# Kernel tuning notes

Measured on AMD Instinct MI355X. Metric: run time of the kernel, lower is better.

The kernel has to match this reference:

```python
import jax, jax.numpy as jnp
import numpy as np

N_LEVELS_ACT = 256  # 8-bit activations (q, k, v)
N_LEVELS_W = 256    # 8-bit softmax weights (always_zero: zp=0)
GN_GROUPS = 32
GN_EPS = 1e-6


def round_ste(x):
    # straight-through round (identity grad)
    return x + jax.lax.stop_gradient(jnp.round(x) - x)


def fake_quant(x, delta, zp, n_levels):
    xq = jnp.clip(round_ste(x / delta) + zp, 0.0, n_levels - 1)
    return (xq - zp) * delta


def group_norm(x, gamma, beta):
    b, c, h, w = x.shape
    xg = x.reshape(b, GN_GROUPS, c // GN_GROUPS, h, w)
    mu = jnp.mean(xg, axis=(2, 3, 4), keepdims=True)
    var = jnp.var(xg, axis=(2, 3, 4), keepdims=True)
    xg = (xg - mu) * jax.lax.rsqrt(var + GN_EPS)
    x = xg.reshape(b, c, h, w)
    return x * gamma[None, :, None, None] + beta[None, :, None, None]


def conv1x1(x, w, b):
    # x: [b,c,h,w], w: [out,in]
    return jnp.einsum('oc,bchw->bohw', w, x) + b[None, :, None, None]


def setup_inputs() -> dict:
    key = jax.random.key(0)
    ks = jax.random.split(key, 8)
    B, C, H, W = 4, 512, 64, 64
    s = 1.0 / np.sqrt(C)
    inp = {
        'x': jax.random.normal(ks[0], (B, C, H, W), jnp.float32),
        'gamma': jnp.ones((C,), jnp.float32),
        'beta': jnp.zeros((C,), jnp.float32),
        'wq': jax.random.normal(ks[1], (C, C), jnp.float32) * s,
        'bq': jnp.zeros((C,), jnp.float32),
        'wk': jax.random.normal(ks[2], (C, C), jnp.float32) * s,
        'bk': jnp.zeros((C,), jnp.float32),
        'wv': jax.random.normal(ks[3], (C, C), jnp.float32) * s,
        'bv': jnp.zeros((C,), jnp.float32),
        'wp': jax.random.normal(ks[4], (C, C), jnp.float32) * s,
        'bp': jnp.zeros((C,), jnp.float32),
        # calibrated asymmetric 8-bit ranges ~ [-4, 4] for q/k/v
        'delta_q': jnp.float32(8.0 / 255.0), 'zp_q': jnp.float32(128.0),
        'delta_k': jnp.float32(8.0 / 255.0), 'zp_k': jnp.float32(128.0),
        'delta_v': jnp.float32(8.0 / 255.0), 'zp_v': jnp.float32(128.0),
        # softmax weights in [0,1], always_zero => zp=0, delta = max/(2^b-1)
        'delta_w': jnp.float32(1.0 / 255.0),
    }
    return inp


def reference(x, gamma, beta, wq, bq, wk, bk, wv, bv, wp, bp,
              delta_q, zp_q, delta_k, zp_k, delta_v, zp_v, delta_w):
    b, c, h, w = x.shape
    hn = group_norm(x, gamma, beta)
    q = conv1x1(hn, wq, bq).reshape(b, c, h * w).transpose(0, 2, 1)  # [b,hw,c]
    k = conv1x1(hn, wk, bk).reshape(b, c, h * w)                      # [b,c,hw]
    v = conv1x1(hn, wv, bv).reshape(b, c, h * w)                      # [b,c,hw]
    q = fake_quant(q, delta_q, zp_q, N_LEVELS_ACT)
    k = fake_quant(k, delta_k, zp_k, N_LEVELS_ACT)
    w_ = jnp.einsum('bqc,bck->bqk', q, k) * (float(c) ** -0.5)
    w_ = jax.nn.softmax(w_, axis=2)
    w_ = w_.transpose(0, 2, 1)  # [b,k,q]
    v = fake_quant(v, delta_v, zp_v, N_LEVELS_ACT)
    w_ = fake_quant(w_, delta_w, jnp.float32(0.0), N_LEVELS_W)
    h_ = jnp.einsum('bck,bkq->bcq', v, w_).reshape(b, c, h, w)
    h_ = conv1x1(h_, wp, bp)
    return x + h_
```

## Files before the change

### kernel.cpp

```cpp
#include <hip/hip_runtime.h>
#include <cstdint>
#include <cstddef>

#define B_  4
#define C_  512
#define HW_ 4096

typedef unsigned short u16t;
typedef signed char s8t;
typedef __attribute__((ext_vector_type(8))) __bf16 bf16x8;
typedef __attribute__((ext_vector_type(4))) float  f32x4;
typedef __attribute__((ext_vector_type(4))) int    i32x4;

__device__ __forceinline__ u16t f2bft(float f) {
    return (u16t)(__float_as_uint(f) >> 16);
}
__device__ __forceinline__ float bf2f(u16t h) {
    return __uint_as_float(((unsigned int)h) << 16);
}
__device__ __forceinline__ f32x4 mfma16(bf16x8 a, bf16x8 b, f32x4 c) {
    return __builtin_amdgcn_mfma_f32_16x16x32_bf16(a, b, c, 0, 0, 0);
}
__device__ __forceinline__ i32x4 mfma_i8(i32x4 a, i32x4 b, i32x4 c) {
    return __builtin_amdgcn_mfma_i32_16x16x64_i8(a, b, c, 0, 0, 0);
}
__device__ __forceinline__ void gl16(const void* g, void* l) {
    __builtin_amdgcn_global_load_lds(
        (__attribute__((address_space(1))) unsigned int*)g,
        (__attribute__((address_space(3))) unsigned int*)l, 16, 0, 0);
}

__global__ __launch_bounds__(256) void split_w(
    const float* __restrict__ wq_, const float* __restrict__ wk_,
    const float* __restrict__ wv_, const float* __restrict__ wp_,
    u16t* __restrict__ out)
{
    int i = blockIdx.x * 256 + threadIdx.x;
    int mat = i >> 18, idx = i & 262143;
    const float* src = (mat == 0) ? wq_ : (mat == 1) ? wk_ : (mat == 2) ? wv_ : wp_;
    float v = src[idx];
    u16t hi = f2bft(v);
    u16t lo = f2bft(v - bf2f(hi));
    out[(size_t)mat * 524288 + idx] = hi;
    out[(size_t)mat * 524288 + 262144 + idx] = lo;
}

__global__ __launch_bounds__(1024) void gn_stats(
    const float* __restrict__ x, float2* __restrict__ stats)
{
    const int tid = threadIdx.x;
    const int bg = blockIdx.x;
    const int b = bg >> 5, g = bg & 31;
    const float4* x4 = (const float4*)(x + ((size_t)b * C_ + g * 16) * HW_);
    float s = 0.f, s2 = 0.f;
    for (int i = tid; i < 16384; i += 1024) {
        float4 v = x4[i];
        s  += v.x + v.y + v.z + v.w;
        s2 += v.x * v.x + v.y * v.y + v.z * v.z + v.w * v.w;
    }
    for (int off = 32; off; off >>= 1) { s += __shfl_down(s, off); s2 += __shfl_down(s2, off); }
    __shared__ float rs[16], rs2[16];
    int w = tid >> 6, lane = tid & 63;
    if (lane == 0) { rs[w] = s; rs2[w] = s2; }
    __syncthreads();
    if (tid == 0) {
        float S = 0.f, S2 = 0.f;
        #pragma unroll
        for (int i = 0; i < 16; ++i) { S += rs[i]; S2 += rs2[i]; }
        float mu = S * (1.f / 65536.f);
        float var = S2 * (1.f / 65536.f) - mu * mu;
        stats[bg] = make_float2(mu, 1.f / sqrtf(var + 1e-6f));
    }
}

__global__ __launch_bounds__(256) void gn_apply(
    const float* __restrict__ x, const float* __restrict__ gamma,
    const float* __restrict__ beta, const float2* __restrict__ stats,
    u16t* __restrict__ hn_hi, u16t* __restrict__ hn_lo)
{
    __shared__ unsigned int tile[16 * 529];
    __shared__ float sa[512], sb[512];
    const int tid = threadIdx.x;
    const int b = blockIdx.y, p0 = blockIdx.x * 16;
    for (int c = tid; c < 512; c += 256) {
        float2 st = stats[b * 32 + (c >> 4)];
        float a = st.y * gamma[c];
        sa[c] = a; sb[c] = beta[c] - st.x * a;
    }
    __syncthreads();
    const float4* x4 = (const float4*)(x + (size_t)b * C_ * HW_);
    const int f4 = tid & 3, cb = tid >> 2;
    #pragma unroll
    for (int it = 0; it < 8; ++it) {
        int c = cb + it * 64;
        float4 v = x4[(size_t)c * (HW_ / 4) + (p0 >> 2) + f4];
        float a = sa[c], bo = sb[c];
        float ys[4] = { v.x, v.y, v.z, v.w };
        #pragma unroll
        for (int j = 0; j < 4; ++j) {
            float y = ys[j] * a + bo;
            u16t hi = f2bft(y);
            u16t lo = f2bft(y - bf2f(hi));
            tile[(f4 * 4 + j) * 529 + c] = (unsigned int)hi | ((unsigned int)lo << 16);
        }
    }
    __syncthreads();
    const int p = tid & 15, seg = tid >> 4;
    size_t ro = ((size_t)b * HW_ + p0 + p) * C_;
    #pragma unroll
    for (int gg = 0; gg < 4; ++gg) {
        const unsigned int* src = &tile[p * 529 + seg * 32 + gg * 8];
        uint4 va = *(const uint4*)src;
        uint4 vb = *(const uint4*)(src + 4);
        uint4 hi4, lo4;
        hi4.x = (va.x & 0xFFFFu) | (va.y << 16);
        hi4.y = (va.z & 0xFFFFu) | (va.w << 16);
        hi4.z = (vb.x & 0xFFFFu) | (vb.y << 16);
        hi4.w = (vb.z & 0xFFFFu) | (vb.w << 16);
        lo4.x = (va.x >> 16) | (va.y & 0xFFFF0000u);
        lo4.y = (va.z >> 16) | (va.w & 0xFFFF0000u);
        lo4.z = (vb.x >> 16) | (vb.y & 0xFFFF0000u);
        lo4.w = (vb.z >> 16) | (vb.w & 0xFFFF0000u);
        *(uint4*)(hn_hi + ro + seg * 32 + gg * 8) = hi4;
        *(uint4*)(hn_lo + ro + seg * 32 + gg * 8) = lo4;
    }
}

template<int MODE>
__global__ __launch_bounds__(256) void gemm512(
    const u16t* __restrict__ Ahi, const u16t* __restrict__ Alo,
    const u16t* __restrict__ Bhi, const u16t* __restrict__ Blo,
    const float* __restrict__ bias, const float* __restrict__ delta,
    const float* __restrict__ zp, s8t* __restrict__ outq,
    float* __restrict__ outf, const float* __restrict__ resid)
{
    __shared__ __align__(16) u16t lds[16384];
    const int tid = threadIdx.x, w = tid >> 6, lane = tid & 63;
    const int lr = lane & 15, gq = lane >> 4, wr = w >> 1, wc = w & 1;
    const int m0 = blockIdx.x * 128, n0 = blockIdx.y * 128, b = blockIdx.z;
    const size_t boff = (size_t)b * HW_ * C_;
    const u16t* gsrc = (w == 0) ? Ahi : (w == 1) ? Alo : (w == 2) ? (Bhi + boff) : (Blo + boff);
    const int rb0 = (w < 2) ? m0 : n0;
    u16t* ldst = lds + w * 4096;
    const int srow = lane >> 2, sch = lane & 3;
    const u16t* sAh = lds; const u16t* sAl = lds + 4096;
    const u16t* sBh = lds + 8192; const u16t* sBl = lds + 12288;
    f32x4 acc[4][4] = {};

    for (int kt = 0; kt < 16; ++kt) {
        const u16t* gk = gsrc + (size_t)(rb0 + srow) * C_ + kt * 32 + sch * 8;
        #pragma unroll
        for (int i = 0; i < 8; ++i) gl16(gk + i * 16 * C_, ldst + i * 512);
        __syncthreads();
        bf16x8 ah[4], al[4], bh[4], bl[4];
        #pragma unroll
        for (int m = 0; m < 4; ++m) {
            int r = wr * 64 + m * 16 + lr;
            ah[m] = *(const bf16x8*)(sAh + r * 32 + gq * 8);
            al[m] = *(const bf16x8*)(sAl + r * 32 + gq * 8);
        }
        #pragma unroll
        for (int n = 0; n < 4; ++n) {
            int r = wc * 64 + n * 16 + lr;
            bh[n] = *(const bf16x8*)(sBh + r * 32 + gq * 8);
            bl[n] = *(const bf16x8*)(sBl + r * 32 + gq * 8);
        }
        #pragma unroll
        for (int m = 0; m < 4; ++m)
            #pragma unroll
            for (int n = 0; n < 4; ++n) {
                acc[m][n] = mfma16(ah[m], bh[n], acc[m][n]);
                acc[m][n] = mfma16(ah[m], bl[n], acc[m][n]);
                acc[m][n] = mfma16(al[m], bh[n], acc[m][n]);
            }
        __syncthreads();
    }

    if constexpr (MODE == 0) {
        const float d = *delta, z = *zp;
        const float rd = 1.0f / d;
        char* T8 = (char*)lds;
        #pragma unroll
        for (int m = 0; m < 4; ++m)
            #pragma unroll
            for (int n = 0; n < 4; ++n)
                #pragma unroll
                for (int j = 0; j < 4; ++j) {
                    int row = wr * 64 + m * 16 + gq * 4 + j;
                    int col = wc * 64 + n * 16 + lr;
                    float val = acc[m][n][j] + bias[m0 + row];
                    float q = fminf(fmaxf(rintf(val * rd), -z), 255.f - z);
                    T8[col * 144 + row] = (char)(int)q;
                }
        __syncthreads();
        int pl = tid >> 1, hf = tid & 1;
        uint4* dst = (uint4*)(outq + ((size_t)b * HW_ + n0 + pl) * C_ + m0 + hf * 64);
        const uint4* s4 = (const uint4*)(T8 + pl * 144 + hf * 64);
        #pragma unroll
        for (int i = 0; i < 4; ++i) dst[i] = s4[i];
    } else if constexpr (MODE == 1) {
        const float d = *delta, z = *zp;
        const float rd = 1.0f / d;
        char* T8 = (char*)lds;
        #pragma unroll
        for (int m = 0; m < 4; ++m)
            #pragma unroll
            for (int n = 0; n < 4; ++n)
                #pragma unroll
                for (int j = 0; j < 4; ++j) {
                    int row = wr * 64 + m * 16 + gq * 4 + j;
                    int col = wc * 64 + n * 16 + lr;
                    float val = acc[m][n][j] + bias[m0 + row];
                    float q = fminf(fmaxf(rintf(val * rd), -z), 255.f - z);
                    T8[row * 144 + col] = (char)(int)q;
                }
        __syncthreads();
        int pl = tid >> 1, hf = tid & 1;
        uint4* dst = (uint4*)(outq + ((size_t)b * C_ + m0 + pl) * HW_ + n0 + hf * 64);
        const uint4* s4 = (const uint4*)(T8 + pl * 144 + hf * 64);
        #pragma unroll
        for (int i = 0; i < 4; ++i) dst[i] = s4[i];
    } else {
        #pragma unroll
        for (int m = 0; m < 4; ++m)
            #pragma unroll
            for (int n = 0; n < 4; ++n)
                #pragma unroll
                for (int j = 0; j < 4; ++j) {
                    int row = wr * 64 + m * 16 + gq * 4 + j;
                    int col = wc * 64 + n * 16 + lr;
                    size_t o = ((size_t)b * C_ + m0 + row) * HW_ + n0 + col;
                    outf[o] = acc[m][n][j] + bias[m0 + row] + resid[o];
                }
    }
}

template<int PASS>
__global__ __launch_bounds__(256) void attn_score(
    const s8t* __restrict__ Qt, const s8t* __restrict__ Kt,
    const float* __restrict__ dqp, const float* __restrict__ dkp,
    float2* __restrict__ pml, const float2* __restrict__ ml,
    s8t* __restrict__ W8)
{
    __shared__ __align__(16) char lds[18432];
    __shared__ float redm[256], reds[256];
    const int tid = threadIdx.x, w = tid >> 6, lane = tid & 63;
    const int lr = lane & 15, gq = lane >> 4, wr = w >> 1, wc = w & 1;
    const int m0 = blockIdx.x * 128, n0 = blockIdx.y * 128, b = blockIdx.z;
    const size_t bo = (size_t)b * HW_ * C_;
    const s8t* gsrc = ((w < 2) ? Qt : Kt) + bo;
    const int rb0 = ((w < 2) ? m0 : n0) + (w & 1) * 64;
    char* ldst = lds + ((w < 2) ? 0 : 8192) + (w & 1) * 4096;
    const int srow = lane >> 2, sch = lane & 3;
    i32x4 acc[4][4] = {};

    for (int kt = 0; kt < 8; ++kt) {
        const s8t* gk = gsrc + (size_t)(rb0 + srow) * C_ + kt * 64 + sch * 16;
        #pragma unroll
        for (int i = 0; i < 4; ++i) gl16(gk + (size_t)i * 16 * C_, ldst + i * 1024);
        __syncthreads();
        i32x4 af[4], bf[4];
        #pragma unroll
        for (int m = 0; m < 4; ++m)
            af[m] = *(const i32x4*)(lds + (wr * 64 + m * 16 + lr) * 64 + gq * 16);
        #pragma unroll
        for (int n = 0; n < 4; ++n)
            bf[n] = *(const i32x4*)(lds + 8192 + (wc * 64 + n * 16 + lr) * 64 + gq * 16);
        #pragma unroll
        for (int m = 0; m < 4; ++m)
            #pragma unroll
            for (int n = 0; n < 4; ++n)
                acc[m][n] = mfma_i8(af[m], bf[n], acc[m][n]);
        __syncthreads();
    }

    const float sc = (*dqp) * (*dkp) * 0.044194173824159216f;
    if constexpr (PASS == 0) {
        #pragma unroll
        for (int m = 0; m < 4; ++m)
            #pragma unroll
            for (int j = 0; j < 4; ++j) {
                float v0 = (float)acc[m][0][j] * sc, v1 = (float)acc[m][1][j] * sc;
                float v2 = (float)acc[m][2][j] * sc, v3 = (float)acc[m][3][j] * sc;
                float mx = fmaxf(fmaxf(v0, v1), fmaxf(v2, v3));
                for (int off = 1; off < 16; off <<= 1) mx = fmaxf(mx, __shfl_xor(mx, off));
                float se = __expf(v0 - mx) + __expf(v1 - mx) + __expf(v2 - mx) + __expf(v3 - mx);
                for (int off = 1; off < 16; off <<= 1) se += __shfl_xor(se, off);
                if (lr == 0) {
                    int r = wr * 64 + m * 16 + gq * 4 + j;
                    redm[r * 2 + wc] = mx; reds[r * 2 + wc] = se;
                }
            }
        __syncthreads();
        if (tid < 128) {
            float ma = redm[tid * 2], mb = redm[tid * 2 + 1];
            float mm = fmaxf(ma, mb);
            float ss = reds[tid * 2] * __expf(ma - mm) + reds[tid * 2 + 1] * __expf(mb - mm);
            pml[((size_t)b * HW_ + m0 + tid) * 32 + blockIdx.y] = make_float2(mm, ss);
        }
    } else {
        char* P8 = lds;
        #pragma unroll
        for (int m = 0; m < 4; ++m)
            #pragma unroll
            for (int j = 0; j < 4; ++j) {
                int row = wr * 64 + m * 16 + gq * 4 + j;
                float2 mv = ml[(size_t)b * HW_ + m0 + row];
                #pragma unroll
                for (int n = 0; n < 4; ++n) {
                    int col = wc * 64 + n * 16 + lr;
                    float sv = __builtin_fmaf((float)acc[m][n][j], sc, -mv.x);
                    float r = rintf(__expf(sv) * mv.y);
                    r = fminf(fmaxf(r, 0.f), 255.f);
                    P8[row * 144 + col] = (char)((int)r - 128);
                }
            }
        __syncthreads();
        int pl = tid >> 1, hf = tid & 1;
        uint4* dst = (uint4*)(W8 + ((size_t)b * HW_ + m0 + pl) * HW_ + n0 + hf * 64);
        const uint4* s4 = (const uint4*)(P8 + pl * 144 + hf * 64);
        #pragma unroll
        for (int i = 0; i < 4; ++i) dst[i] = s4[i];
    }
}

__global__ __launch_bounds__(256) void reduce_ml_k(
    const float2* __restrict__ pml, float2* __restrict__ ml,
    const float* __restrict__ dwp)
{
    int idx = blockIdx.x * 256 + threadIdx.x;
    const float2* p = pml + (size_t)idx * 32;
    float2 vv[32];
    float mm = -3.402823466e38f;
    #pragma unroll
    for (int i = 0; i < 32; ++i) { vv[i] = p[i]; mm = fmaxf(mm, vv[i].x); }
    float l = 0.f;
    #pragma unroll
    for (int i = 0; i < 32; ++i) l += vv[i].y * __expf(vv[i].x - mm);
    ml[idx] = make_float2(mm, 1.0f / (l * (*dwp)));
}

__global__ __launch_bounds__(64) void rowsum_v(
    const s8t* __restrict__ V, int* __restrict__ rsum)
{
    const int row = blockIdx.x, lane = threadIdx.x;
    const int4* src = (const int4*)(V + (size_t)row * HW_);
    int s = 0;
    #pragma unroll
    for (int it = 0; it < 4; ++it) {
        int4 v = src[it * 64 + lane];
        int ww[4] = { v.x, v.y, v.z, v.w };
        #pragma unroll
        for (int d = 0; d < 4; ++d) {
            int xv = ww[d];
            s += (int)(s8t)(xv) + (int)(s8t)(xv >> 8)
               + (int)(s8t)(xv >> 16) + (int)(s8t)(xv >> 24);
        }
    }
    #pragma unroll
    for (int off = 32; off; off >>= 1) s += __shfl_down(s, off);
    if (lane == 0) rsum[row] = s;
}

__global__ __launch_bounds__(256) void pv_kernel(
    const s8t* __restrict__ V, const s8t* __restrict__ W8,
    const int* __restrict__ rsum,
    const float* __restrict__ dvp, const float* __restrict__ dwp,
    u16t* __restrict__ h_hi, u16t* __restrict__ h_lo)
{
    __shared__ __align__(16) char lds[34816];
    const int tid = threadIdx.x, w = tid >> 6, lane = tid & 63;
    const int lr = lane & 15, gq = lane >> 4, wr = w >> 1, wc = w & 1;
    const int m0 = blockIdx.x * 128, n0 = blockIdx.y * 128, b = blockIdx.z;
    const int srow = lane >> 2, sch = lane & 3;
    const s8t* gbase = (w < 2)
        ? (V  + ((size_t)(b * C_  + m0 + (w & 1) * 64 + srow)) * HW_)
        : (W8 + ((size_t)b * HW_ + n0 + (w & 1) * 64 + srow) * HW_);
    char* ldst = lds + ((w < 2) ? 0 : 8192) + (w & 1) * 4096;
    i32x4 acc[4][4] = {};

    for (int kt = 0; kt < 64; ++kt) {
        const s8t* gk = gbase + kt * 64 + sch * 16;
        #pragma unroll
        for (int i = 0; i < 4; ++i) gl16(gk + (size_t)i * 16 * HW_, ldst + i * 1024);
        __syncthreads();
        i32x4 af[4], bf[4];
        #pragma unroll
        for (int m = 0; m < 4; ++m)
            af[m] = *(const i32x4*)(lds + (wr * 64 + m * 16 + lr) * 64 + gq * 16);
        #pragma unroll
        for (int n = 0; n < 4; ++n)
            bf[n] = *(const i32x4*)(lds + 8192 + (wc * 64 + n * 16 + lr) * 64 + gq * 16);
        #pragma unroll
        for (int m = 0; m < 4; ++m)
            #pragma unroll
            for (int n = 0; n < 4; ++n)
                acc[m][n] = mfma_i8(af[m], bf[n], acc[m][n]);
        __syncthreads();
    }

    const float scl = (*dvp) * (*dwp);
    int rsv[4][4];
    #pragma unroll
    for (int m = 0; m < 4; ++m)
        #pragma unroll
        for (int j = 0; j < 4; ++j)
            rsv[m][j] = rsum[(size_t)b * C_ + m0 + wr * 64 + m * 16 + gq * 4 + j];

    u16t* T = (u16t*)lds;
    #pragma unroll
    for (int m = 0; m < 4; ++m)
        #pragma unroll
        for (int n = 0; n < 4; ++n)
            #pragma unroll
            for (int j = 0; j < 4; ++j) {
                int row = wr * 64 + m * 16 + gq * 4 + j;
                int col = wc * 64 + n * 16 + lr;
                float h = (float)(acc[m][n][j] + 128 * rsv[m][j]) * scl;
                T[col * 136 + row] = f2bft(h);
            }
    __syncthreads();
    {
        int pl = tid >> 1, hf = tid & 1;
        uint4* dst = (uint4*)(h_hi + ((size_t)b * HW_ + n0 + pl) * C_ + m0 + hf * 64);
        const uint4* s4 = (const uint4*)(T + pl * 136 + hf * 64);
        #pragma unroll
        for (int i = 0; i < 8; ++i) dst[i] = s4[i];
    }
    __syncthreads();
    #pragma unroll
    for (int m = 0; m < 4; ++m)
        #pragma unroll
        for (int n = 0; n < 4; ++n)
            #pragma unroll
            for (int j = 0; j < 4; ++j) {
                int row = wr * 64 + m * 16 + gq * 4 + j;
                int col = wc * 64 + n * 16 + lr;
                float h = (float)(acc[m][n][j] + 128 * rsv[m][j]) * scl;
                u16t hi = f2bft(h);
                T[col * 136 + row] = f2bft(h - bf2f(hi));
            }
    __syncthreads();
    {
        int pl = tid >> 1, hf = tid & 1;
        uint4* dst = (uint4*)(h_lo + ((size_t)b * HW_ + n0 + pl) * C_ + m0 + hf * 64);
        const uint4* s4 = (const uint4*)(T + pl * 136 + hf * 64);
        #pragma unroll
        for (int i = 0; i < 8; ++i) dst[i] = s4[i];
    }
}

extern "C" void kernel_launch(void* const* d_in, const int* in_sizes, int n_in,
                              void* d_out, int out_size, void* d_ws, size_t ws_size,
                              hipStream_t stream)
{
    const float* x     = (const float*)d_in[0];
    const float* gamma = (const float*)d_in[1];
    const float* beta  = (const float*)d_in[2];
    const float* wq = (const float*)d_in[3];
    const float* bq = (const float*)d_in[4];
    const float* wk = (const float*)d_in[5];
    const float* bk = (const float*)d_in[6];
    const float* wv = (const float*)d_in[7];
    const float* bv = (const float*)d_in[8];
    const float* wp = (const float*)d_in[9];
    const float* bp = (const float*)d_in[10];
    const float* dq = (const float*)d_in[11];
    const float* zq = (const float*)d_in[12];
    const float* dk = (const float*)d_in[13];
    const float* zk = (const float*)d_in[14];
    const float* dv = (const float*)d_in[15];
    const float* zv = (const float*)d_in[16];
    const float* dw = (const float*)d_in[17];
    float* out = (float*)d_out;
    char* ws = (char*)d_ws;
    const size_t MiB = 1048576;

    u16t* wsp   = (u16t*)ws;
    s8t*  Vq    = (s8t*)(ws + 4 * MiB);
    s8t*  W8    = (s8t*)(ws + 12 * MiB);
    u16t* hn_hi = (u16t*)(ws + 12 * MiB);
    u16t* hn_lo = (u16t*)(ws + 28 * MiB);
    float2* pml = (float2*)(ws + 44 * MiB);
    s8t*  Qt    = (s8t*)(ws + 76 * MiB);
    s8t*  Kt    = (s8t*)(ws + 84 * MiB);
    u16t* hh    = (u16t*)(ws + 76 * MiB);
    u16t* hl    = (u16t*)(ws + 92 * MiB);
    float2* ml  = (float2*)(ws + 108 * MiB);
    int*  rsum  = (int*)(ws + 108 * MiB + 131072);
    float2* stats = (float2*)(ws + 108 * MiB + 131072 + 8192);
    if (ws_size < 108 * MiB + 131072 + 8192 + 1024) return;

    dim3 blk(256);
    split_w<<<dim3(4096), blk, 0, stream>>>(wq, wk, wv, wp, wsp);
    gn_stats<<<dim3(128), dim3(1024), 0, stream>>>(x, stats);
    gn_apply<<<dim3(256, 4), blk, 0, stream>>>(x, gamma, beta, stats, hn_hi, hn_lo);
    dim3 gg(4, 32, 4);
    gemm512<0><<<gg, blk, 0, stream>>>(wsp + 0,       wsp + 262144,  hn_hi, hn_lo, bq, dq, zq, Qt, nullptr, nullptr);
    gemm512<0><<<gg, blk, 0, stream>>>(wsp + 524288,  wsp + 786432,  hn_hi, hn_lo, bk, dk, zk, Kt, nullptr, nullptr);
    gemm512<1><<<gg, blk, 0, stream>>>(wsp + 1048576, wsp + 1310720, hn_hi, hn_lo, bv, dv, zv, Vq, nullptr, nullptr);
    rowsum_v<<<dim3(2048), dim3(64), 0, stream>>>(Vq, rsum);
    dim3 ga(32, 32, 4);
    attn_score<0><<<ga, blk, 0, stream>>>(Qt, Kt, dq, dk, pml, nullptr, nullptr);
    reduce_ml_k<<<dim3(64), blk, 0, stream>>>(pml, ml, dw);
    attn_score<1><<<ga, blk, 0, stream>>>(Qt, Kt, dq, dk, nullptr, ml, W8);
    pv_kernel<<<gg, blk, 0, stream>>>(Vq, W8, rsum, dv, dw, hh, hl);
    gemm512<2><<<gg, blk, 0, stream>>>(wsp + 1572864, wsp + 1835008, hh, hl, bp, nullptr, nullptr, nullptr, out, x);
}
```

Measured before the change: 485.2 us.

## Double-buffer LDS loads in attention kernels and enlarge score tile rows

Both attention score passes and the PV GEMM now prefetch the next K-slice into a second LDS buffer while MFMAs run on the current one, dropping one barrier per iteration. The attention score kernel also grows its tile from 128 to 256 query rows per block, so each K tile is reused twice as often. The grid is halved to match, and the softmax-stat and quantised-weight epilogues are extended to the larger tile. The cost is more LDS (48 KB) and higher accumulator register pressure in attn_score, which may lower occupancy.

```diff
diff --git a/kernel.cpp b/kernel.cpp
--- a/kernel.cpp
+++ b/kernel.cpp
@@ -236,48 +236,62 @@
 }
 
 template<int PASS>
-__global__ __launch_bounds__(256) void attn_score(
+__global__ __launch_bounds__(256, 2) void attn_score(
     const s8t* __restrict__ Qt, const s8t* __restrict__ Kt,
     const float* __restrict__ dqp, const float* __restrict__ dkp,
     float2* __restrict__ pml, const float2* __restrict__ ml,
     s8t* __restrict__ W8)
 {
-    __shared__ __align__(16) char lds[18432];
-    __shared__ float redm[256], reds[256];
+    __shared__ __align__(16) char lds[49152];
+    __shared__ float redm[512], reds[512];
     const int tid = threadIdx.x, w = tid >> 6, lane = tid & 63;
     const int lr = lane & 15, gq = lane >> 4, wr = w >> 1, wc = w & 1;
-    const int m0 = blockIdx.x * 128, n0 = blockIdx.y * 128, b = blockIdx.z;
+    const int m0 = blockIdx.x * 256, n0 = blockIdx.y * 128, b = blockIdx.z;
     const size_t bo = (size_t)b * HW_ * C_;
-    const s8t* gsrc = ((w < 2) ? Qt : Kt) + bo;
-    const int rb0 = ((w < 2) ? m0 : n0) + (w & 1) * 64;
-    char* ldst = lds + ((w < 2) ? 0 : 8192) + (w & 1) * 4096;
     const int srow = lane >> 2, sch = lane & 3;
-    i32x4 acc[4][4] = {};
-
+    const s8t* Abase = Qt + bo + (size_t)(m0 + w * 64 + srow) * C_ + sch * 16;
+    const s8t* Bbase = Kt + bo + (size_t)(n0 + w * 32 + srow) * C_ + sch * 16;
+    char* Adst = lds + (w * 64) * 64;
+    char* Bdst = lds + 16384 + (w * 32) * 64;
+    i32x4 acc[8][4] = {};
+
+    #pragma unroll
+    for (int i = 0; i < 4; ++i) gl16(Abase + (size_t)i * 16 * C_, Adst + i * 1024);
+    #pragma unroll
+    for (int i = 0; i < 2; ++i) gl16(Bbase + (size_t)i * 16 * C_, Bdst + i * 1024);
+    __syncthreads();
+    int cur = 0;
     for (int kt = 0; kt < 8; ++kt) {
-        const s8t* gk = gsrc + (size_t)(rb0 + srow) * C_ + kt * 64 + sch * 16;
-        #pragma unroll
-        for (int i = 0; i < 4; ++i) gl16(gk + (size_t)i * 16 * C_, ldst + i * 1024);
-        __syncthreads();
-        i32x4 af[4], bf[4];
-        #pragma unroll
-        for (int m = 0; m < 4; ++m)
-            af[m] = *(const i32x4*)(lds + (wr * 64 + m * 16 + lr) * 64 + gq * 16);
+        if (kt < 7) {
+            int koff = (kt + 1) * 64;
+            char* ad = Adst + (cur ^ 1) * 24576;
+            char* bd = Bdst + (cur ^ 1) * 24576;
+            #pragma unroll
+            for (int i = 0; i < 4; ++i) gl16(Abase + koff + (size_t)i * 16 * C_, ad + i * 1024);
+            #pragma unroll
+            for (int i = 0; i < 2; ++i) gl16(Bbase + koff + (size_t)i * 16 * C_, bd + i * 1024);
+        }
+        const char* rb = lds + cur * 24576;
+        i32x4 a[8], bb[4];
+        #pragma unroll
+        for (int m = 0; m < 8; ++m)
+            a[m] = *(const i32x4*)(rb + (wr * 128 + m * 16 + lr) * 64 + gq * 16);
         #pragma unroll
         for (int n = 0; n < 4; ++n)
-            bf[n] = *(const i32x4*)(lds + 8192 + (wc * 64 + n * 16 + lr) * 64 + gq * 16);
-        #pragma unroll
-        for (int m = 0; m < 4; ++m)
+            bb[n] = *(const i32x4*)(rb + 16384 + (wc * 64 + n * 16 + lr) * 64 + gq * 16);
+        #pragma unroll
+        for (int m = 0; m < 8; ++m)
             #pragma unroll
             for (int n = 0; n < 4; ++n)
-                acc[m][n] = mfma_i8(af[m], bf[n], acc[m][n]);
-        __syncthreads();
+                acc[m][n] = mfma_i8(a[m], bb[n], acc[m][n]);
+        __syncthreads();
+        cur ^= 1;
     }
 
     const float sc = (*dqp) * (*dkp) * 0.044194173824159216f;
     if constexpr (PASS == 0) {
         #pragma unroll
-        for (int m = 0; m < 4; ++m)
+        for (int m = 0; m < 8; ++m)
             #pragma unroll
             for (int j = 0; j < 4; ++j) {
                 float v0 = (float)acc[m][0][j] * sc, v1 = (float)acc[m][1][j] * sc;
@@ -287,12 +301,12 @@
                 float se = __expf(v0 - mx) + __expf(v1 - mx) + __expf(v2 - mx) + __expf(v3 - mx);
                 for (int off = 1; off < 16; off <<= 1) se += __shfl_xor(se, off);
                 if (lr == 0) {
-                    int r = wr * 64 + m * 16 + gq * 4 + j;
+                    int r = wr * 128 + m * 16 + gq * 4 + j;
                     redm[r * 2 + wc] = mx; reds[r * 2 + wc] = se;
                 }
             }
         __syncthreads();
-        if (tid < 128) {
+        {
             float ma = redm[tid * 2], mb = redm[tid * 2 + 1];
             float mm = fmaxf(ma, mb);
             float ss = reds[tid * 2] * __expf(ma - mm) + reds[tid * 2 + 1] * __expf(mb - mm);
@@ -301,10 +315,10 @@
     } else {
         char* P8 = lds;
         #pragma unroll
-        for (int m = 0; m < 4; ++m)
+        for (int m = 0; m < 8; ++m)
             #pragma unroll
             for (int j = 0; j < 4; ++j) {
-                int row = wr * 64 + m * 16 + gq * 4 + j;
+                int row = wr * 128 + m * 16 + gq * 4 + j;
                 float2 mv = ml[(size_t)b * HW_ + m0 + row];
                 #pragma unroll
                 for (int n = 0; n < 4; ++n) {
@@ -317,10 +331,13 @@
             }
         __syncthreads();
         int pl = tid >> 1, hf = tid & 1;
-        uint4* dst = (uint4*)(W8 + ((size_t)b * HW_ + m0 + pl) * HW_ + n0 + hf * 64);
-        const uint4* s4 = (const uint4*)(P8 + pl * 144 + hf * 64);
-        #pragma unroll
-        for (int i = 0; i < 4; ++i) dst[i] = s4[i];
+        #pragma unroll
+        for (int h = 0; h < 2; ++h) {
+            uint4* dst = (uint4*)(W8 + ((size_t)b * HW_ + m0 + h * 128 + pl) * HW_ + n0 + hf * 64);
+            const uint4* s4 = (const uint4*)(P8 + (h * 128 + pl) * 144 + hf * 64);
+            #pragma unroll
+            for (int i = 0; i < 4; ++i) dst[i] = s4[i];
+        }
     }
 }
 
@@ -379,24 +396,35 @@
     char* ldst = lds + ((w < 2) ? 0 : 8192) + (w & 1) * 4096;
     i32x4 acc[4][4] = {};
 
+    {
+        const s8t* gk = gbase + sch * 16;
+        #pragma unroll
+        for (int i = 0; i < 4; ++i) gl16(gk + (size_t)i * 16 * HW_, ldst + i * 1024);
+    }
+    __syncthreads();
+    int cur = 0;
     for (int kt = 0; kt < 64; ++kt) {
-        const s8t* gk = gbase + kt * 64 + sch * 16;
-        #pragma unroll
-        for (int i = 0; i < 4; ++i) gl16(gk + (size_t)i * 16 * HW_, ldst + i * 1024);
-        __syncthreads();
+        if (kt < 63) {
+            const s8t* gk = gbase + (kt + 1) * 64 + sch * 16;
+            char* nd = ldst + (cur ^ 1) * 16384;
+            #pragma unroll
+            for (int i = 0; i < 4; ++i) gl16(gk + (size_t)i * 16 * HW_, nd + i * 1024);
+        }
+        const char* rb = lds + cur * 16384;
         i32x4 af[4], bf[4];
         #pragma unroll
         for (int m = 0; m < 4; ++m)
-            af[m] = *(const i32x4*)(lds + (wr * 64 + m * 16 + lr) * 64 + gq * 16);
+            af[m] = *(const i32x4*)(rb + (wr * 64 + m * 16 + lr) * 64 + gq * 16);
         #pragma unroll
         for (int n = 0; n < 4; ++n)
-            bf[n] = *(const i32x4*)(lds + 8192 + (wc * 64 + n * 16 + lr) * 64 + gq * 16);
+            bf[n] = *(const i32x4*)(rb + 8192 + (wc * 64 + n * 16 + lr) * 64 + gq * 16);
         #pragma unroll
         for (int m = 0; m < 4; ++m)
             #pragma unroll
             for (int n = 0; n < 4; ++n)
                 acc[m][n] = mfma_i8(af[m], bf[n], acc[m][n]);
         __syncthreads();
+        cur ^= 1;
     }
 
     const float scl = (*dvp) * (*dwp);
@@ -500,7 +528,7 @@
     gemm512<0><<<gg, blk, 0, stream>>>(wsp + 524288,  wsp + 786432,  hn_hi, hn_lo, bk, dk, zk, Kt, nullptr, nullptr);
     gemm512<1><<<gg, blk, 0, stream>>>(wsp + 1048576, wsp + 1310720, hn_hi, hn_lo, bv, dv, zv, Vq, nullptr, nullptr);
     rowsum_v<<<dim3(2048), dim3(64), 0, stream>>>(Vq, rsum);
-    dim3 ga(32, 32, 4);
+    dim3 ga(16, 32, 4);
     attn_score<0><<<ga, blk, 0, stream>>>(Qt, Kt, dq, dk, pml, nullptr, nullptr);
     reduce_ml_k<<<dim3(64), blk, 0, stream>>>(pml, ml, dw);
     attn_score<1><<<ga, blk, 0, stream>>>(Qt, Kt, dq, dk, nullptr, ml, W8);
```

New measurement: 490.5 us. About the same (+1.1%).

## Merge Q/K/V projection GEMMs into one launch and double-buffer PV kernel loads

Applied to the files above, without the earlier changes.

The three separate Q, K and V projection GEMM launches become a single kernel whose grid is three times wider, with a block index selecting the weight, bias and quantization parameters. This cuts launch overhead and gives more blocks in flight per wave. The PV kernel now ping-pongs between two LDS buffers, so the next K-tile's global-to-LDS load is issued before the current tile's MFMAs. That drops one barrier per iteration and overlaps memory with compute, at the cost of doubling the LDS footprint, which may reduce occupancy.

```diff
diff --git a/kernel.cpp b/kernel.cpp
--- a/kernel.cpp
+++ b/kernel.cpp
@@ -126,12 +126,114 @@
     }
 }
 
-template<int MODE>
-__global__ __launch_bounds__(256) void gemm512(
+__global__ __launch_bounds__(256) void qkv_gemm(
+    const u16t* __restrict__ wsp,
+    const u16t* __restrict__ Bhi, const u16t* __restrict__ Blo,
+    const float* __restrict__ bq_, const float* __restrict__ bk_,
+    const float* __restrict__ bv_,
+    const float* __restrict__ dq_, const float* __restrict__ zq_,
+    const float* __restrict__ dk_, const float* __restrict__ zk_,
+    const float* __restrict__ dv_, const float* __restrict__ zv_,
+    s8t* __restrict__ Qt, s8t* __restrict__ Kt, s8t* __restrict__ Vq)
+{
+    __shared__ __align__(16) u16t lds[16384];
+    const int tid = threadIdx.x, w = tid >> 6, lane = tid & 63;
+    const int lr = lane & 15, gq = lane >> 4, wr = w >> 1, wc = w & 1;
+    const int mat = blockIdx.x >> 2;
+    const int m0 = (blockIdx.x & 3) * 128, n0 = blockIdx.y * 128, b = blockIdx.z;
+    const size_t boff = (size_t)b * HW_ * C_;
+    const u16t* Ahi = wsp + (size_t)mat * 524288;
+    const u16t* Alo = Ahi + 262144;
+    const u16t* gsrc = (w == 0) ? Ahi : (w == 1) ? Alo : (w == 2) ? (Bhi + boff) : (Blo + boff);
+    const int rb0 = (w < 2) ? m0 : n0;
+    u16t* ldst = lds + w * 4096;
+    const int srow = lane >> 2, sch = lane & 3;
+    const u16t* sAh = lds; const u16t* sAl = lds + 4096;
+    const u16t* sBh = lds + 8192; const u16t* sBl = lds + 12288;
+    f32x4 acc[4][4] = {};
+
+    for (int kt = 0; kt < 16; ++kt) {
+        const u16t* gk = gsrc + (size_t)(rb0 + srow) * C_ + kt * 32 + sch * 8;
+        #pragma unroll
+        for (int i = 0; i < 8; ++i) gl16(gk + i * 16 * C_, ldst + i * 512);
+        __syncthreads();
+        bf16x8 ah[4], al[4], bh[4], bl[4];
+        #pragma unroll
+        for (int m = 0; m < 4; ++m) {
+            int r = wr * 64 + m * 16 + lr;
+            ah[m] = *(const bf16x8*)(sAh + r * 32 + gq * 8);
+            al[m] = *(const bf16x8*)(sAl + r * 32 + gq * 8);
+        }
+        #pragma unroll
+        for (int n = 0; n < 4; ++n) {
+            int r = wc * 64 + n * 16 + lr;
+            bh[n] = *(const bf16x8*)(sBh + r * 32 + gq * 8);
+            bl[n] = *(const bf16x8*)(sBl + r * 32 + gq * 8);
+        }
+        #pragma unroll
+        for (int m = 0; m < 4; ++m)
+            #pragma unroll
+            for (int n = 0; n < 4; ++n) {
+                acc[m][n] = mfma16(ah[m], bh[n], acc[m][n]);
+                acc[m][n] = mfma16(ah[m], bl[n], acc[m][n]);
+                acc[m][n] = mfma16(al[m], bh[n], acc[m][n]);
+            }
+        __syncthreads();
+    }
+
+    const float* bias = (mat == 0) ? bq_ : (mat == 1) ? bk_ : bv_;
+    const float d = (mat == 0) ? *dq_ : (mat == 1) ? *dk_ : *dv_;
+    const float z = (mat == 0) ? *zq_ : (mat == 1) ? *zk_ : *zv_;
+    const float rd = 1.0f / d;
+    s8t* outq = (mat == 0) ? Qt : (mat == 1) ? Kt : Vq;
+
+    if (mat < 2) {
+        char* T8 = (char*)lds;
+        #pragma unroll
+        for (int m = 0; m < 4; ++m)
+            #pragma unroll
+            for (int n = 0; n < 4; ++n)
+                #pragma unroll
+                for (int j = 0; j < 4; ++j) {
+                    int row = wr * 64 + m * 16 + gq * 4 + j;
+                    int col = wc * 64 + n * 16 + lr;
+                    float val = acc[m][n][j] + bias[m0 + row];
+                    float q = fminf(fmaxf(rintf(val * rd), -z), 255.f - z);
+                    T8[col * 144 + row] = (char)(int)q;
+                }
+        __syncthreads();
+        int pl = tid >> 1, hf = tid & 1;
+        uint4* dst = (uint4*)(outq + ((size_t)b * HW_ + n0 + pl) * C_ + m0 + hf * 64);
+        const uint4* s4 = (const uint4*)(T8 + pl * 144 + hf * 64);
+        #pragma unroll
+        for (int i = 0; i < 4; ++i) dst[i] = s4[i];
+    } else {
+        char* T8 = (char*)lds;
+        #pragma unroll
+        for (int m = 0; m < 4; ++m)
+            #pragma unroll
+            for (int n = 0; n < 4; ++n)
+                #pragma unroll
+                for (int j = 0; j < 4; ++j) {
+                    int row = wr * 64 + m * 16 + gq * 4 + j;
+                    int col = wc * 64 + n * 16 + lr;
+                    float val = acc[m][n][j] + bias[m0 + row];
+                    float q = fminf(fmaxf(rintf(val * rd), -z), 255.f - z);
+                    T8[row * 144 + col] = (char)(int)q;
+                }
+        __syncthreads();
+        int pl = tid >> 1, hf = tid & 1;
+        uint4* dst = (uint4*)(outq + ((size_t)b * C_ + m0 + pl) * HW_ + n0 + hf * 64);
+        const uint4* s4 = (const uint4*)(T8 + pl * 144 + hf * 64);
+        #pragma unroll
+        for (int i = 0; i < 4; ++i) dst[i] = s4[i];
+    }
+}
+
+__global__ __launch_bounds__(256) void proj_gemm(
     const u16t* __restrict__ Ahi, const u16t* __restrict__ Alo,
     const u16t* __restrict__ Bhi, const u16t* __restrict__ Blo,
-    const float* __restrict__ bias, const float* __restrict__ delta,
-    const float* __restrict__ zp, s8t* __restrict__ outq,
+    const float* __restrict__ bias,
     float* __restrict__ outf, const float* __restrict__ resid)
 {
     __shared__ __align__(16) u16t lds[16384];
@@ -176,63 +278,17 @@
         __syncthreads();
     }
 
-    if constexpr (MODE == 0) {
-        const float d = *delta, z = *zp;
-        const float rd = 1.0f / d;
-        char* T8 = (char*)lds;
-        #pragma unroll
-        for (int m = 0; m < 4; ++m)
-            #pragma unroll
-            for (int n = 0; n < 4; ++n)
-                #pragma unroll
-                for (int j = 0; j < 4; ++j) {
-                    int row = wr * 64 + m * 16 + gq * 4 + j;
-                    int col = wc * 64 + n * 16 + lr;
-                    float val = acc[m][n][j] + bias[m0 + row];
-                    float q = fminf(fmaxf(rintf(val * rd), -z), 255.f - z);
-                    T8[col * 144 + row] = (char)(int)q;
-                }
-        __syncthreads();
-        int pl = tid >> 1, hf = tid & 1;
-        uint4* dst = (uint4*)(outq + ((size_t)b * HW_ + n0 + pl) * C_ + m0 + hf * 64);
-        const uint4* s4 = (const uint4*)(T8 + pl * 144 + hf * 64);
-        #pragma unroll
-        for (int i = 0; i < 4; ++i) dst[i] = s4[i];
-    } else if constexpr (MODE == 1) {
-        const float d = *delta, z = *zp;
-        const float rd = 1.0f / d;
-        char* T8 = (char*)lds;
-        #pragma unroll
-        for (int m = 0; m < 4; ++m)
-            #pragma unroll
-            for (int n = 0; n < 4; ++n)
-                #pragma unroll
-                for (int j = 0; j < 4; ++j) {
-                    int row = wr * 64 + m * 16 + gq * 4 + j;
-                    int col = wc * 64 + n * 16 + lr;
-                    float val = acc[m][n][j] + bias[m0 + row];
-                    float q = fminf(fmaxf(rintf(val * rd), -z), 255.f - z);
-                    T8[row * 144 + col] = (char)(int)q;
-                }
-        __syncthreads();
-        int pl = tid >> 1, hf = tid & 1;
-        uint4* dst = (uint4*)(outq + ((size_t)b * C_ + m0 + pl) * HW_ + n0 + hf * 64);
-        const uint4* s4 = (const uint4*)(T8 + pl * 144 + hf * 64);
-        #pragma unroll
-        for (int i = 0; i < 4; ++i) dst[i] = s4[i];
-    } else {
-        #pragma unroll
-        for (int m = 0; m < 4; ++m)
-            #pragma unroll
-            for (int n = 0; n < 4; ++n)
-                #pragma unroll
-                for (int j = 0; j < 4; ++j) {
-                    int row = wr * 64 + m * 16 + gq * 4 + j;
-                    int col = wc * 64 + n * 16 + lr;
-                    size_t o = ((size_t)b * C_ + m0 + row) * HW_ + n0 + col;
-                    outf[o] = acc[m][n][j] + bias[m0 + row] + resid[o];
-                }
-    }
+    #pragma unroll
+    for (int m = 0; m < 4; ++m)
+        #pragma unroll
+        for (int n = 0; n < 4; ++n)
+            #pragma unroll
+            for (int j = 0; j < 4; ++j) {
+                int row = wr * 64 + m * 16 + gq * 4 + j;
+                int col = wc * 64 + n * 16 + lr;
+                size_t o = ((size_t)b * C_ + m0 + row) * HW_ + n0 + col;
+                outf[o] = acc[m][n][j] + bias[m0 + row] + resid[o];
+            }
 }
 
 template<int PASS>
@@ -379,24 +435,35 @@
     char* ldst = lds + ((w < 2) ? 0 : 8192) + (w & 1) * 4096;
     i32x4 acc[4][4] = {};
 
+    {
+        const s8t* gk = gbase + sch * 16;
+        #pragma unroll
+        for (int i = 0; i < 4; ++i) gl16(gk + (size_t)i * 16 * HW_, ldst + i * 1024);
+    }
+    __syncthreads();
+    int cur = 0;
     for (int kt = 0; kt < 64; ++kt) {
-        const s8t* gk = gbase + kt * 64 + sch * 16;
-        #pragma unroll
-        for (int i = 0; i < 4; ++i) gl16(gk + (size_t)i * 16 * HW_, ldst + i * 1024);
-        __syncthreads();
+        if (kt < 63) {
+            const s8t* gk = gbase + (kt + 1) * 64 + sch * 16;
+            char* nd = ldst + (cur ^ 1) * 16384;
+            #pragma unroll
+            for (int i = 0; i < 4; ++i) gl16(gk + (size_t)i * 16 * HW_, nd + i * 1024);
+        }
+        const char* rb = lds + cur * 16384;
         i32x4 af[4], bf[4];
         #pragma unroll
         for (int m = 0; m < 4; ++m)
-            af[m] = *(const i32x4*)(lds + (wr * 64 + m * 16 + lr) * 64 + gq * 16);
+            af[m] = *(const i32x4*)(rb + (wr * 64 + m * 16 + lr) * 64 + gq * 16);
         #pragma unroll
         for (int n = 0; n < 4; ++n)
-            bf[n] = *(const i32x4*)(lds + 8192 + (wc * 64 + n * 16 + lr) * 64 + gq * 16);
+            bf[n] = *(const i32x4*)(rb + 8192 + (wc * 64 + n * 16 + lr) * 64 + gq * 16);
         #pragma unroll
         for (int m = 0; m < 4; ++m)
             #pragma unroll
             for (int n = 0; n < 4; ++n)
                 acc[m][n] = mfma_i8(af[m], bf[n], acc[m][n]);
         __syncthreads();
+        cur ^= 1;
     }
 
     const float scl = (*dvp) * (*dwp);
@@ -495,15 +562,14 @@
     split_w<<<dim3(4096), blk, 0, stream>>>(wq, wk, wv, wp, wsp);
     gn_stats<<<dim3(128), dim3(1024), 0, stream>>>(x, stats);
     gn_apply<<<dim3(256, 4), blk, 0, stream>>>(x, gamma, beta, stats, hn_hi, hn_lo);
-    dim3 gg(4, 32, 4);
-    gemm512<0><<<gg, blk, 0, stream>>>(wsp + 0,       wsp + 262144,  hn_hi, hn_lo, bq, dq, zq, Qt, nullptr, nullptr);
-    gemm512<0><<<gg, blk, 0, stream>>>(wsp + 524288,  wsp + 786432,  hn_hi, hn_lo, bk, dk, zk, Kt, nullptr, nullptr);
-    gemm512<1><<<gg, blk, 0, stream>>>(wsp + 1048576, wsp + 1310720, hn_hi, hn_lo, bv, dv, zv, Vq, nullptr, nullptr);
+    qkv_gemm<<<dim3(12, 32, 4), blk, 0, stream>>>(
+        wsp, hn_hi, hn_lo, bq, bk, bv, dq, zq, dk, zk, dv, zv, Qt, Kt, Vq);
     rowsum_v<<<dim3(2048), dim3(64), 0, stream>>>(Vq, rsum);
     dim3 ga(32, 32, 4);
     attn_score<0><<<ga, blk, 0, stream>>>(Qt, Kt, dq, dk, pml, nullptr, nullptr);
     reduce_ml_k<<<dim3(64), blk, 0, stream>>>(pml, ml, dw);
     attn_score<1><<<ga, blk, 0, stream>>>(Qt, Kt, dq, dk, nullptr, ml, W8);
+    dim3 gg(4, 32, 4);
     pv_kernel<<<gg, blk, 0, stream>>>(Vq, W8, rsum, dv, dw, hh, hl);
-    gemm512<2><<<gg, blk, 0, stream>>>(wsp + 1572864, wsp + 1835008, hh, hl, bp, nullptr, nullptr, nullptr, out, x);
-}
+    proj_gemm<<<gg, blk, 0, stream>>>(wsp + 1572864, wsp + 1835008, hh, hl, bp, out, x);
+}
```

After: 452.3 us. 1.07x faster.
